# Kernel optimization log

Hardware: AMD Instinct MI355X
Metric: run time of the kernel (lower is better)

## Reference

```python
import jax, jax.numpy as jnp
import numpy as np

N_NODES = 100000
N_EDGES = 3200000
F_IN, F_HID, F_OUT = 25, 16, 2


def gcn_conv(x, edge_index, W, b, n_nodes):
    """PyG GCNConv: out = D^-1/2 (A + I) D^-1/2 (x W) + b."""
    h = x @ W  # [N, F_out] transform first (small feature dim)
    loops = jnp.arange(n_nodes, dtype=edge_index.dtype)
    row = jnp.concatenate([edge_index[0], loops])  # sources j
    col = jnp.concatenate([edge_index[1], loops])  # targets i
    ones = jnp.ones(row.shape[0], dtype=h.dtype)
    deg = jax.ops.segment_sum(ones, col, num_segments=n_nodes)
    dinv = jnp.where(deg > 0, jax.lax.rsqrt(jnp.maximum(deg, 1.0)), 0.0)
    norm = dinv[row] * dinv[col]  # [E+N]
    msgs = h[row] * norm[:, None]  # gather + scale
    out = jax.ops.segment_sum(msgs, col, num_segments=n_nodes)
    return out + b


def setup_inputs() -> dict:
    key = jax.random.key(0)
    k1, k2, k3, k4, k5, k6 = jax.random.split(key, 6)
    x = jax.random.normal(k1, (N_NODES, F_IN), dtype=jnp.float32)
    edge_index = jax.random.randint(k2, (2, N_EDGES), 0, N_NODES, dtype=jnp.int64)
    s1 = 1.0 / np.sqrt(F_IN)
    s2 = 1.0 / np.sqrt(F_HID)
    W1 = jax.random.uniform(k3, (F_IN, F_HID), jnp.float32, -s1, s1)
    b1 = jax.random.uniform(k4, (F_HID,), jnp.float32, -s1, s1)
    W2 = jax.random.uniform(k5, (F_HID, F_OUT), jnp.float32, -s2, s2)
    b2 = jax.random.uniform(k6, (F_OUT,), jnp.float32, -s2, s2)
    return {"x": x, "edge_index": edge_index, "W1": W1, "b1": b1, "W2": W2, "b2": b2}


def reference(x, edge_index, W1, b1, W2, b2):
    n = x.shape[0]
    h = jax.nn.relu(gcn_conv(x, edge_index, W1, b1, n))
    h = gcn_conv(h, edge_index, W2, b2, n)
    return jax.nn.log_softmax(h, axis=1)
```

## Files before the change

### kernel.cpp

```cpp
#include <hip/hip_runtime.h>
#include <hip/hip_fp16.h>
#include <math.h>

#define THREADS 256
#define NPB 512
#define SHIFT 9
#define MASK 511
#define MAX_BINS 256
#define CAPE 18432
#define BIN_BLOCKS 512


__global__ void __launch_bounds__(256) k_bin(const int* __restrict__ row,
                                             const int* __restrict__ col,
                                             int e, int* __restrict__ binCnt,
                                             int* __restrict__ binned) {
    __shared__ int hist[MAX_BINS];
    __shared__ int cur[MAX_BINS];
    __shared__ int baseg[MAX_BINS];
    __shared__ int lofs[MAX_BINS];
    __shared__ int scn[MAX_BINS];
    extern __shared__ int dyn[];
    int per = (((e + (int)gridDim.x - 1) / (int)gridDim.x) + 3) & ~3;
    int e0 = blockIdx.x * per;
    if (e0 >= e) return;
    int e1 = min(e0 + per, e);
    int cntL = e1 - e0;
    int* sbuf  = dyn;
    int* sbuf2 = dyn + per;
    unsigned char* sbin = (unsigned char*)(dyn + 2 * per);
    int tid = threadIdx.x;
    hist[tid] = 0; cur[tid] = 0;
    __syncthreads();
    int nq = cntL >> 2;
    const int4* r4 = (const int4*)(row + e0);
    const int4* c4 = (const int4*)(col + e0);
    for (int q = tid; q < nq; q += 256) {
        int4 r = r4[q], c = c4[q];
        int b0 = c.x >> SHIFT, b1 = c.y >> SHIFT, b2 = c.z >> SHIFT, b3 = c.w >> SHIFT;
        ((int4*)sbuf)[q] = make_int4((r.x << SHIFT) | (c.x & MASK),
                                     (r.y << SHIFT) | (c.y & MASK),
                                     (r.z << SHIFT) | (c.z & MASK),
                                     (r.w << SHIFT) | (c.w & MASK));
        *((uchar4*)(sbin + q * 4)) = make_uchar4((unsigned char)b0, (unsigned char)b1,
                                                 (unsigned char)b2, (unsigned char)b3);
        atomicAdd(&hist[b0], 1); atomicAdd(&hist[b1], 1);
        atomicAdd(&hist[b2], 1); atomicAdd(&hist[b3], 1);
    }
    for (int li = (nq << 2) + tid; li < cntL; li += 256) {
        int c = col[e0 + li], r = row[e0 + li], b = c >> SHIFT;
        sbuf[li] = (r << SHIFT) | (c & MASK);
        sbin[li] = (unsigned char)b;
        atomicAdd(&hist[b], 1);
    }
    __syncthreads();
    {
        int h = hist[tid];
        baseg[tid] = (h > 0) ? atomicAdd(&binCnt[tid], h) : 0;
        scn[tid] = h;
    }
    __syncthreads();
    for (int off = 1; off < MAX_BINS; off <<= 1) {
        int a = (tid >= off) ? scn[tid - off] : 0;
        __syncthreads();
        scn[tid] += a;
        __syncthreads();
    }
    lofs[tid] = scn[tid] - hist[tid];
    __syncthreads();
    for (int li = tid; li < cntL; li += 256) {
        int b = sbin[li];
        int p = lofs[b] + atomicAdd(&cur[b], 1);
        sbuf2[p] = sbuf[li];
    }
    __syncthreads();
    int wv = tid >> 6, ln = tid & 63;
    for (int b = wv; b < MAX_BINS; b += 4) {
        int len = hist[b];
        int lo = lofs[b];
        int gb = baseg[b];
        for (int i = ln; i < len; i += 64) {
            int pos = gb + i;
            if (pos < CAPE) binned[b * CAPE + pos] = sbuf2[lo + i];
        }
    }
}


__global__ void __launch_bounds__(512) k_sort(const int* __restrict__ binned,
                                              const int* __restrict__ binCnt,
                                              int* __restrict__ csr,
                                              int* __restrict__ gptr,
                                              int* __restrict__ gcnt,
                                              float* __restrict__ dinv, int n) {
    __shared__ int cnt[NPB];
    __shared__ int scn[NPB];
    int b = blockIdx.x;
    int t = threadIdx.x;
    cnt[t] = 0;
    __syncthreads();
    int m = min(binCnt[b], CAPE);
    const int* eb = binned + b * CAPE;
    for (int i = t; i < m; i += 512)
        atomicAdd(&cnt[eb[i] & MASK], 1);
    __syncthreads();
    int v = cnt[t];
    scn[t] = v;
    __syncthreads();
    for (int off = 1; off < NPB; off <<= 1) {
        int a = (t >= off) ? scn[t - off] : 0;
        __syncthreads();
        scn[t] += a;
        __syncthreads();
    }
    int excl = scn[t] - v;
    int node = b * NPB + t;
    if (node < n) {
        gptr[node] = b * CAPE + excl;
        gcnt[node] = v;
        dinv[node] = rsqrtf((float)(v + 1));
    }
    cnt[t] = excl;
    __syncthreads();
    for (int i = t; i < m; i += 512) {
        int e = eb[i];
        int slot = atomicAdd(&cnt[e & MASK], 1);
        csr[b * CAPE + slot] = e >> SHIFT;
    }
}

__global__ void __launch_bounds__(256) k_xform1(const float* __restrict__ x,
                                                const float* __restrict__ W1,
                                                const float* __restrict__ dinv,
                                                __half* __restrict__ z1h, int n) {
    __shared__ float sW[25 * 16];
    __shared__ float tile[4][64 * 25];
    int w = threadIdx.x >> 6, lane = threadIdx.x & 63;
    for (int t = threadIdx.x; t < 25 * 16; t += 256) sW[t] = W1[t];
    long blockRow = (long)blockIdx.x * 256;
    long waveRow = blockRow + w * 64;
    const float* src = x + waveRow * 25;
    long rem = (long)n * 25 - waveRow * 25;
#pragma unroll
    for (int k = 0; k < 25; k++) {
        int idx = k * 64 + lane;
        tile[w][idx] = (idx < rem) ? src[idx] : 0.f;
    }
    __syncthreads();
    long node = blockRow + threadIdx.x;
    if (node >= n) return;
    float xi[25];
#pragma unroll
    for (int k = 0; k < 25; k++) xi[k] = tile[w][lane * 25 + k];
    float di = dinv[node];
    union { int4 v[2]; __half h[16]; } u;
#pragma unroll
    for (int c = 0; c < 16; c++) {
        float a = 0.f;
#pragma unroll
        for (int k = 0; k < 25; k++) a = fmaf(xi[k], sW[k * 16 + c], a);
        u.h[c] = __float2half(a * di);
    }
    int4* o = (int4*)(z1h + node * 16);
    o[0] = u.v[0];
    o[1] = u.v[1];
}

__global__ void k_gather1(const int* __restrict__ ptr, const int* __restrict__ cnt,
                          const int* __restrict__ csr, const __half* __restrict__ z1h,
                          const float* __restrict__ dinv,
                          const float* __restrict__ b1, const float* __restrict__ W2,
                          __half2* __restrict__ z2h, int n) {
    int g = threadIdx.x >> 3;
    int c2 = threadIdx.x & 7;
    int node = blockIdx.x * 32 + g;
    if (node >= n) return;
    const __half2* z1p = (const __half2*)z1h;
    int beg = ptr[node], d = cnt[node];
    __half2 sv = z1p[(size_t)node * 8 + c2];
    float a0 = __low2float(sv), a1 = __high2float(sv);
    int e = 0;
    for (; e + 4 <= d; e += 4) {
        int s0 = csr[beg + e], s1 = csr[beg + e + 1];
        int s2 = csr[beg + e + 2], s3 = csr[beg + e + 3];
        __half2 v0 = z1p[(size_t)s0 * 8 + c2];
        __half2 v1 = z1p[(size_t)s1 * 8 + c2];
        __half2 v2 = z1p[(size_t)s2 * 8 + c2];
        __half2 v3 = z1p[(size_t)s3 * 8 + c2];
        a0 += (__low2float(v0) + __low2float(v1)) + (__low2float(v2) + __low2float(v3));
        a1 += (__high2float(v0) + __high2float(v1)) + (__high2float(v2) + __high2float(v3));
    }
    for (; e < d; e++) {
        __half2 v = z1p[(size_t)csr[beg + e] * 8 + c2];
        a0 += __low2float(v);
        a1 += __high2float(v);
    }
    float di = dinv[node];
    int cA = c2 * 2, cB = c2 * 2 + 1;
    float hA = fmaxf(fmaf(di, a0, b1[cA]), 0.f);
    float hB = fmaxf(fmaf(di, a1, b1[cB]), 0.f);
    float p0 = hA * W2[cA * 2 + 0] + hB * W2[cB * 2 + 0];
    float p1 = hA * W2[cA * 2 + 1] + hB * W2[cB * 2 + 1];
#pragma unroll
    for (int m = 1; m < 8; m <<= 1) {
        p0 += __shfl_xor(p0, m, 8);
        p1 += __shfl_xor(p1, m, 8);
    }
    if (c2 == 0) z2h[node] = __floats2half2_rn(di * p0, di * p1);
}

__global__ void k_gather2(const int* __restrict__ ptr, const int* __restrict__ cnt,
                          const int* __restrict__ csr, const __half2* __restrict__ z2h,
                          const float* __restrict__ dinv,
                          const float* __restrict__ b2, float* __restrict__ out, int n) {
    int g = threadIdx.x >> 3;
    int c = threadIdx.x & 7;
    int node = blockIdx.x * 32 + g;
    if (node >= n) return;
    int beg = ptr[node], d = cnt[node];
    float a0 = 0.f, a1 = 0.f;
    for (int e = c; e < d; e += 8) {
        __half2 v = z2h[csr[beg + e]];
        a0 += __low2float(v);
        a1 += __high2float(v);
    }
#pragma unroll
    for (int m = 1; m < 8; m <<= 1) {
        a0 += __shfl_xor(a0, m, 8);
        a1 += __shfl_xor(a1, m, 8);
    }
    if (c == 0) {
        __half2 self = z2h[node];
        a0 += __low2float(self);
        a1 += __high2float(self);
        float di = dinv[node];
        float h0 = fmaf(di, a0, b2[0]);
        float h1 = fmaf(di, a1, b2[1]);
        float mx = fmaxf(h0, h1);
        float lse = mx + log1pf(expf(fminf(h0, h1) - mx));
        ((float2*)out)[node] = make_float2(h0 - lse, h1 - lse);
    }
}


__global__ void k_zero(int* cnt, int n) {
    int i = blockIdx.x * blockDim.x + threadIdx.x;
    if (i < n) cnt[i] = 0;
}

__global__ void k_count_pos(const int* __restrict__ col, int e,
                            int* __restrict__ cnt, int* __restrict__ pos) {
    int i = blockIdx.x * blockDim.x + threadIdx.x;
    if (i < e) pos[i] = atomicAdd(&cnt[col[i]], 1);
}

__global__ void k_scan1(const int* __restrict__ cnt, int n,
                        int* __restrict__ excl, int* __restrict__ bsum) {
    __shared__ int s[256];
    int i = blockIdx.x * 256 + threadIdx.x;
    int v = (i < n) ? cnt[i] : 0;
    s[threadIdx.x] = v;
    __syncthreads();
    for (int off = 1; off < 256; off <<= 1) {
        int t = (threadIdx.x >= off) ? s[threadIdx.x - off] : 0;
        __syncthreads();
        s[threadIdx.x] += t;
        __syncthreads();
    }
    if (i < n) excl[i] = s[threadIdx.x] - v;
    if (threadIdx.x == 255) bsum[blockIdx.x] = s[255];
}

__global__ void k_scan2(int* __restrict__ bsum, int nb) {
    __shared__ int s[1024];
    int v = (threadIdx.x < nb) ? bsum[threadIdx.x] : 0;
    s[threadIdx.x] = v;
    __syncthreads();
    for (int off = 1; off < 1024; off <<= 1) {
        int t = (threadIdx.x >= off) ? s[threadIdx.x - off] : 0;
        __syncthreads();
        s[threadIdx.x] += t;
        __syncthreads();
    }
    if (threadIdx.x < nb) bsum[threadIdx.x] = s[threadIdx.x] - v;
}

__global__ void k_scan3(int* __restrict__ excl, const int* __restrict__ boff, int n) {
    int i = blockIdx.x * 256 + threadIdx.x;
    if (i < n) excl[i] += boff[blockIdx.x];
}

__global__ void k_place(const int* __restrict__ row, const int* __restrict__ col,
                        const int* __restrict__ pos, const int* __restrict__ ptr,
                        int e, int* __restrict__ csr) {
    int i = blockIdx.x * blockDim.x + threadIdx.x;
    if (i >= e) return;
    csr[ptr[col[i]] + pos[i]] = row[i];
}

__global__ void k_dinv_from_cnt(const int* __restrict__ cnt, float* __restrict__ dinv, int n) {
    int i = blockIdx.x * blockDim.x + threadIdx.x;
    if (i < n) dinv[i] = rsqrtf((float)(cnt[i] + 1));
}


extern "C" void kernel_launch(void* const* d_in, const int* in_sizes, int n_in,
                              void* d_out, int out_size, void* d_ws, size_t ws_size,
                              hipStream_t stream) {
    const float* x  = (const float*)d_in[0];
    const int*   ei = (const int*)d_in[1];
    const float* W1 = (const float*)d_in[2];
    const float* b1 = (const float*)d_in[3];
    const float* W2 = (const float*)d_in[4];
    const float* b2 = (const float*)d_in[5];
    float* out = (float*)d_out;

    const int N = in_sizes[0] / 25;
    const int E = in_sizes[1] / 2;
    const int* row = ei;
    const int* col = ei + E;

    const int nbins = (N + NPB - 1) / NPB;
    const int gN = (N + THREADS - 1) / THREADS;
    const int gE = (E + THREADS - 1) / THREADS;

    size_t off = 0;
    auto take = [&](size_t bytes) { size_t o = off; off = (off + bytes + 255) & ~(size_t)255; return o; };
    size_t o_binCnt = take(MAX_BINS * sizeof(int));
    size_t o_binned = take((size_t)nbins * CAPE * sizeof(int));
    size_t o_csr    = take((size_t)nbins * CAPE * sizeof(int));
    size_t o_ptr    = take((size_t)N * sizeof(int));
    size_t o_cnt    = take((size_t)N * sizeof(int));
    size_t o_dinv   = take((size_t)N * sizeof(float));
    size_t o_z1h    = take((size_t)N * 16 * sizeof(__half));
    size_t o_z2h    = take((size_t)N * sizeof(__half2));
    size_t need_v11 = off;

    double mu = (double)E / (double)nbins;
    bool cap_ok = (mu + 8.0 * sqrt(mu)) < (double)CAPE;
    const int per = (((E + BIN_BLOCKS - 1) / BIN_BLOCKS) + 3) & ~3;
    size_t dynLds = (size_t)per * 9 + 64;
    bool lds_ok = dynLds <= 60 * 1024;
    bool use_v11 = (nbins <= MAX_BINS) && (ws_size >= need_v11) &&
                   (N <= NPB * MAX_BINS) && cap_ok && lds_ok;

    char* wsb = (char*)d_ws;
    if (use_v11) {
        int*     binCnt = (int*)(wsb + o_binCnt);
        int*     binned = (int*)(wsb + o_binned);
        int*     csr    = (int*)(wsb + o_csr);
        int*     ptr    = (int*)(wsb + o_ptr);
        int*     cnt    = (int*)(wsb + o_cnt);
        float*   dinv   = (float*)(wsb + o_dinv);
        __half*  z1h    = (__half*)(wsb + o_z1h);
        __half2* z2h    = (__half2*)(wsb + o_z2h);

        hipMemsetAsync(binCnt, 0, MAX_BINS * sizeof(int), stream);
        k_bin<<<BIN_BLOCKS, 256, dynLds, stream>>>(row, col, E, binCnt, binned);
        k_sort<<<nbins, 512, 0, stream>>>(binned, binCnt, csr, ptr, cnt, dinv, N);
        k_xform1<<<gN, 256, 0, stream>>>(x, W1, dinv, z1h, N);
        k_gather1<<<(N + 31) / 32, 256, 0, stream>>>(ptr, cnt, csr, z1h, dinv, b1, W2, z2h, N);
        k_gather2<<<(N + 31) / 32, 256, 0, stream>>>(ptr, cnt, csr, z2h, dinv, b2, out, N);
    } else {
        char* w = wsb;
        int*     cnt  = (int*)w;     w += (size_t)N * sizeof(int);
        int*     ptr  = (int*)w;     w += (size_t)N * sizeof(int);
        int*     pos  = (int*)w;     w += (size_t)E * sizeof(int);
        int*     csr  = (int*)w;     w += (size_t)E * sizeof(int);
        int*     bsum = (int*)w;     w += (size_t)1024 * sizeof(int);
        float*   dinv = (float*)w;   w += (size_t)N * sizeof(float);
        __half*  z1h  = (__half*)w;  w += (size_t)N * 16 * sizeof(__half);
        __half2* z2h  = (__half2*)w; w += (size_t)N * sizeof(__half2);
        const int NB = (N + 255) / 256;

        k_zero<<<gN, THREADS, 0, stream>>>(cnt, N);
        k_count_pos<<<gE, THREADS, 0, stream>>>(col, E, cnt, pos);
        k_scan1<<<NB, 256, 0, stream>>>(cnt, N, ptr, bsum);
        k_scan2<<<1, 1024, 0, stream>>>(bsum, NB);
        k_scan3<<<NB, 256, 0, stream>>>(ptr, bsum, N);
        k_place<<<gE, THREADS, 0, stream>>>(row, col, pos, ptr, E, csr);
        k_dinv_from_cnt<<<gN, THREADS, 0, stream>>>(cnt, dinv, N);
        k_xform1<<<gN, 256, 0, stream>>>(x, W1, dinv, z1h, N);
        k_gather1<<<(N + 31) / 32, 256, 0, stream>>>(ptr, cnt, csr, z1h, dinv, b1, W2, z2h, N);
        k_gather2<<<(N + 31) / 32, 256, 0, stream>>>(ptr, cnt, csr, z2h, dinv, b2, out, N);
    }
}
```

Baseline: 196.4 us.

## Flatten bin scatter writes, cooperatively load edge indices, double bin-kernel blocks

The binning kernel now records each reordered element's bin in a second LDS byte array. The per-bin wave loop, which left lanes idle on short bins, becomes a flat loop over all local elements that computes each global destination directly. The bin-kernel grid is doubled to 1024 blocks, so each block holds fewer edges and needs less LDS per block. In the first gather, the 8 lanes of a node group each load one CSR index and broadcast it with shuffles, replacing redundant per-lane index loads at the cost of shuffle overhead and more serialized accumulation.

```diff
diff --git a/kernel.cpp b/kernel.cpp
--- a/kernel.cpp
+++ b/kernel.cpp
@@ -8,7 +8,7 @@
 #define MASK 511
 #define MAX_BINS 256
 #define CAPE 18432
-#define BIN_BLOCKS 512
+#define BIN_BLOCKS 1024
 
 
 __global__ void __launch_bounds__(256) k_bin(const int* __restrict__ row,
@@ -28,7 +28,8 @@
     int cntL = e1 - e0;
     int* sbuf  = dyn;
     int* sbuf2 = dyn + per;
-    unsigned char* sbin = (unsigned char*)(dyn + 2 * per);
+    unsigned char* sbin  = (unsigned char*)(dyn + 2 * per);
+    unsigned char* sbin2 = sbin + per;
     int tid = threadIdx.x;
     hist[tid] = 0; cur[tid] = 0;
     __syncthreads();
@@ -72,17 +73,13 @@
         int b = sbin[li];
         int p = lofs[b] + atomicAdd(&cur[b], 1);
         sbuf2[p] = sbuf[li];
-    }
-    __syncthreads();
-    int wv = tid >> 6, ln = tid & 63;
-    for (int b = wv; b < MAX_BINS; b += 4) {
-        int len = hist[b];
-        int lo = lofs[b];
-        int gb = baseg[b];
-        for (int i = ln; i < len; i += 64) {
-            int pos = gb + i;
-            if (pos < CAPE) binned[b * CAPE + pos] = sbuf2[lo + i];
-        }
+        sbin2[p] = (unsigned char)b;
+    }
+    __syncthreads();
+    for (int p = tid; p < cntL; p += 256) {
+        int b = sbin2[p];
+        int dst = baseg[b] + (p - lofs[b]);
+        if (dst < CAPE) binned[b * CAPE + dst] = sbuf2[p];
     }
 }
 
@@ -179,21 +176,19 @@
     int beg = ptr[node], d = cnt[node];
     __half2 sv = z1p[(size_t)node * 8 + c2];
     float a0 = __low2float(sv), a1 = __high2float(sv);
-    int e = 0;
-    for (; e + 4 <= d; e += 4) {
-        int s0 = csr[beg + e], s1 = csr[beg + e + 1];
-        int s2 = csr[beg + e + 2], s3 = csr[beg + e + 3];
-        __half2 v0 = z1p[(size_t)s0 * 8 + c2];
-        __half2 v1 = z1p[(size_t)s1 * 8 + c2];
-        __half2 v2 = z1p[(size_t)s2 * 8 + c2];
-        __half2 v3 = z1p[(size_t)s3 * 8 + c2];
-        a0 += (__low2float(v0) + __low2float(v1)) + (__low2float(v2) + __low2float(v3));
-        a1 += (__high2float(v0) + __high2float(v1)) + (__high2float(v2) + __high2float(v3));
-    }
-    for (; e < d; e++) {
-        __half2 v = z1p[(size_t)csr[beg + e] * 8 + c2];
-        a0 += __low2float(v);
-        a1 += __high2float(v);
+    for (int e = 0; e < d; e += 8) {
+        int myIdx = e + c2;
+        int myEdge = (myIdx < d) ? csr[beg + myIdx] : 0;
+        int lim = d - e;
+#pragma unroll
+        for (int j = 0; j < 8; j++) {
+            if (j < lim) {
+                int s = __shfl(myEdge, j, 8);
+                __half2 v = z1p[(size_t)s * 8 + c2];
+                a0 += __low2float(v);
+                a1 += __high2float(v);
+            }
+        }
     }
     float di = dinv[node];
     int cA = c2 * 2, cB = c2 * 2 + 1;
@@ -334,18 +329,18 @@
     size_t o_dinv   = take((size_t)N * sizeof(float));
     size_t o_z1h    = take((size_t)N * 16 * sizeof(__half));
     size_t o_z2h    = take((size_t)N * sizeof(__half2));
-    size_t need_v11 = off;
+    size_t need_v12 = off;
 
     double mu = (double)E / (double)nbins;
     bool cap_ok = (mu + 8.0 * sqrt(mu)) < (double)CAPE;
     const int per = (((E + BIN_BLOCKS - 1) / BIN_BLOCKS) + 3) & ~3;
-    size_t dynLds = (size_t)per * 9 + 64;
+    size_t dynLds = (size_t)per * 10 + 64;
     bool lds_ok = dynLds <= 60 * 1024;
-    bool use_v11 = (nbins <= MAX_BINS) && (ws_size >= need_v11) &&
+    bool use_v12 = (nbins <= MAX_BINS) && (ws_size >= need_v12) &&
                    (N <= NPB * MAX_BINS) && cap_ok && lds_ok;
 
     char* wsb = (char*)d_ws;
-    if (use_v11) {
+    if (use_v12) {
         int*     binCnt = (int*)(wsb + o_binCnt);
         int*     binned = (int*)(wsb + o_binned);
         int*     csr    = (int*)(wsb + o_csr);
```

Result: slower. 205.1 us (+4.4%).
